# Performance work log

Hardware: AMD Instinct MI355X
Metric: run time of the kernel (lower is better)

Reference implementation:

```python
import jax, jax.numpy as jnp
import numpy as np

NUM_HEADS = 16
HEAD_DIM = 64  # dim // num_heads


def setup_inputs() -> dict:
    key = jax.random.key(0)
    ks = jax.random.split(key, 4)
    B, N, C = 16, 4096, 1024
    s = 0.02
    x = jax.random.normal(ks[0], (B, N, C), dtype=jnp.float32)
    Wq = jax.random.normal(ks[1], (C, NUM_HEADS * HEAD_DIM), dtype=jnp.float32) * s
    Wkv = jax.random.normal(ks[2], (C, NUM_HEADS * HEAD_DIM * 2), dtype=jnp.float32) * s
    Wproj = jax.random.normal(ks[3], (NUM_HEADS * HEAD_DIM, C), dtype=jnp.float32) * s
    bproj = jnp.zeros((C,), dtype=jnp.float32)
    return {"x": x, "Wq": Wq, "Wkv": Wkv, "Wproj": Wproj, "bproj": bproj}


def reference(x, Wq, Wkv, Wproj, bproj):
    B, N, C = x.shape
    H, D = NUM_HEADS, HEAD_DIM
    scale = D ** (-0.5)
    # k, v projections over the full sequence: [B, N, 2, H, D]
    kv = (x @ Wkv).reshape(B, N, 2, H, D)
    k = kv[:, :, 0]  # [B, N, H, D]
    v = kv[:, :, 1]  # [B, N, H, D]
    # query from CLS token only: [B, 1, H, D]
    q = (x[:, :1, :] @ Wq).reshape(B, 1, H, D)
    # decode-style attention: single query attends over N keys
    attn = jnp.einsum("bqhd,bnhd->bhqn", q * scale, k)  # [B, H, 1, N]
    attn = jax.nn.softmax(attn, axis=-1)
    cls_embed = jnp.einsum("bhqn,bnhd->bqhd", attn, v).reshape(B, 1, H * D)
    return cls_embed @ Wproj + bproj  # [B, 1, C]
```

## Files before the change

kernel.cpp:

```cpp
#include <hip/hip_runtime.h>
#include <cstddef>
#include <cstdint>

#define B_ 16
#define N_ 4096
#define C_ 1024
#define H_ 16
#define D_ 64
#define HD_ 1024

__device__ __forceinline__ void stage16(const float* g, float* l, int lane) {
#if __has_builtin(__builtin_amdgcn_global_load_lds)
  __builtin_amdgcn_global_load_lds(
      (const __attribute__((address_space(1))) void*)g,
      (__attribute__((address_space(3))) void*)l, 16, 0, 0);
#else
  *(float4*)(l + lane * 4) = *(const float4*)g;
#endif
}

__global__ __launch_bounds__(256) void kA(const float* __restrict__ x,
                                          const float* __restrict__ Wq,
                                          const float* __restrict__ Wkv,
                                          float* __restrict__ u) {
  const int b = blockIdx.x >> 4;
  const int h = blockIdx.x & 15;
  __shared__ float xr[C_];
  __shared__ float qp[4][D_];
  __shared__ float qs[D_];
  const float* xb = x + (size_t)b * N_ * C_;
  for (int c = threadIdx.x; c < C_; c += 256) xr[c] = xb[c];
  __syncthreads();
  const int d = threadIdx.x & 63;
  const int part = threadIdx.x >> 6;
  float a = 0.f;
  const float* wq = Wq + h * D_ + d;
  #pragma unroll 4
  for (int c = part * 256; c < part * 256 + 256; ++c)
    a += xr[c] * wq[(size_t)c * HD_];
  qp[part][d] = a;
  __syncthreads();
  if (threadIdx.x < 64) {
    qs[threadIdx.x] = (qp[0][threadIdx.x] + qp[1][threadIdx.x] +
                       qp[2][threadIdx.x] + qp[3][threadIdx.x]) * 0.125f;
  }
  __syncthreads();
  for (int c = threadIdx.x; c < C_; c += 256) {
    const float4* wr = (const float4*)(Wkv + (size_t)c * (2 * HD_) + h * D_);
    float s = 0.f;
    #pragma unroll
    for (int d4 = 0; d4 < 16; ++d4) {
      float4 wv = wr[d4];
      s += wv.x * qs[4 * d4] + wv.y * qs[4 * d4 + 1] +
           wv.z * qs[4 * d4 + 2] + wv.w * qs[4 * d4 + 3];
    }
    u[(size_t)blockIdx.x * C_ + c] = s;
  }
}

__global__ __launch_bounds__(256, 2) void kF(const float* __restrict__ x,
                                             const float* __restrict__ u,
                                             float* __restrict__ wpart,
                                             float* __restrict__ mbuf,
                                             float* __restrict__ lbuf,
                                             int G) {
  const int b = blockIdx.y;
  const int chunk = blockIdx.x;
  const int CH = gridDim.x;
  const int tid = threadIdx.x;
  const int w = tid >> 6;
  const int lane = tid & 63;
  __shared__ float xs[2][8][C_];

  float4 uf[4][4];
  const float* ub = u + (size_t)(b * H_ + w * 4) * C_;
  #pragma unroll
  for (int hh = 0; hh < 4; ++hh)
    #pragma unroll
    for (int q = 0; q < 4; ++q)
      uf[hh][q] = *(const float4*)(ub + (size_t)hh * C_ + q * 256 + lane * 4);

  float4 acc[4][4];
  #pragma unroll
  for (int hh = 0; hh < 4; ++hh)
    #pragma unroll
    for (int q = 0; q < 4; ++q) acc[hh][q] = make_float4(0.f, 0.f, 0.f, 0.f);
  float m[4] = {-1e30f, -1e30f, -1e30f, -1e30f};
  float l[4] = {0.f, 0.f, 0.f, 0.f};

  const float* xb = x + ((size_t)b * N_ + (size_t)chunk * G * 8) * C_;

  #pragma unroll
  for (int r = 0; r < 8; ++r)
    stage16(xb + (size_t)r * C_ + w * 256 + lane * 4, &xs[0][r][w * 256], lane);

  for (int g = 0; g < G; ++g) {
    __syncthreads();
    if (g + 1 < G) {
      const float* xg = xb + (size_t)(g + 1) * 8 * C_;
      const int nb = (g + 1) & 1;
      #pragma unroll
      for (int r = 0; r < 8; ++r)
        stage16(xg + (size_t)r * C_ + w * 256 + lane * 4, &xs[nb][r][w * 256],
                lane);
    }
    const int buf = g & 1;
    #pragma unroll
    for (int r = 0; r < 8; ++r) {
      float4 xq[4];
      #pragma unroll
      for (int q = 0; q < 4; ++q)
        xq[q] = *(const float4*)&xs[buf][r][q * 256 + lane * 4];
      float ph[4];
      #pragma unroll
      for (int hh = 0; hh < 4; ++hh) {
        float a = 0.f;
        #pragma unroll
        for (int q = 0; q < 4; ++q)
          a += xq[q].x * uf[hh][q].x + xq[q].y * uf[hh][q].y +
               xq[q].z * uf[hh][q].z + xq[q].w * uf[hh][q].w;
        ph[hh] = a;
      }
      #pragma unroll
      for (int mask = 1; mask < 64; mask <<= 1) {
        #pragma unroll
        for (int hh = 0; hh < 4; ++hh) ph[hh] += __shfl_xor(ph[hh], mask);
      }
      float mn[4];
      #pragma unroll
      for (int hh = 0; hh < 4; ++hh) mn[hh] = fmaxf(m[hh], ph[hh]);
      if (mn[0] > m[0] || mn[1] > m[1] || mn[2] > m[2] || mn[3] > m[3]) {
        #pragma unroll
        for (int hh = 0; hh < 4; ++hh) {
          const float alpha = __expf(m[hh] - mn[hh]);
          l[hh] *= alpha;
          #pragma unroll
          for (int q = 0; q < 4; ++q) {
            acc[hh][q].x *= alpha; acc[hh][q].y *= alpha;
            acc[hh][q].z *= alpha; acc[hh][q].w *= alpha;
          }
          m[hh] = mn[hh];
        }
      }
      #pragma unroll
      for (int hh = 0; hh < 4; ++hh) {
        const float p = __expf(ph[hh] - m[hh]);
        l[hh] += p;
        #pragma unroll
        for (int q = 0; q < 4; ++q) {
          acc[hh][q].x += p * xq[q].x; acc[hh][q].y += p * xq[q].y;
          acc[hh][q].z += p * xq[q].z; acc[hh][q].w += p * xq[q].w;
        }
      }
    }
  }

  float* wp = wpart + ((size_t)(b * CH + chunk) * H_ + w * 4) * C_;
  #pragma unroll
  for (int hh = 0; hh < 4; ++hh)
    #pragma unroll
    for (int q = 0; q < 4; ++q)
      *(float4*)(wp + (size_t)hh * C_ + q * 256 + lane * 4) = acc[hh][q];
  if (lane == 0) {
    #pragma unroll
    for (int hh = 0; hh < 4; ++hh) {
      mbuf[(b * CH + chunk) * H_ + w * 4 + hh] = m[hh];
      lbuf[(b * CH + chunk) * H_ + w * 4 + hh] = l[hh];
    }
  }
}

__global__ __launch_bounds__(256) void kM(const float* __restrict__ wpart,
                                          const float* __restrict__ mbuf,
                                          const float* __restrict__ lbuf,
                                          float* __restrict__ w, int CH) {
  const int b = blockIdx.x >> 4;
  const int h = blockIdx.x & 15;
  const int t = threadIdx.x;
  __shared__ float alph[64];
  __shared__ float Linv;
  if (t < 64) {
    float mv = (t < CH) ? mbuf[(b * CH + t) * H_ + h] : -1e30f;
    float M = mv;
    #pragma unroll
    for (int mask = 1; mask < 64; mask <<= 1)
      M = fmaxf(M, __shfl_xor(M, mask));
    const float lv = (t < CH) ? lbuf[(b * CH + t) * H_ + h] : 0.f;
    const float a = __expf(mv - M);
    alph[t] = a;
    float L = a * lv;
    #pragma unroll
    for (int mask = 1; mask < 64; mask <<= 1) L += __shfl_xor(L, mask);
    if (t == 0) Linv = 1.f / L;
  }
  __syncthreads();
  float4 sum = make_float4(0.f, 0.f, 0.f, 0.f);
  for (int s = 0; s < CH; ++s) {
    const float a = alph[s];
    const float4 v =
        *(const float4*)(wpart + ((size_t)(b * CH + s) * H_ + h) * C_ + t * 4);
    sum.x += a * v.x; sum.y += a * v.y; sum.z += a * v.z; sum.w += a * v.w;
  }
  const float li = Linv;
  float4 o = make_float4(sum.x * li, sum.y * li, sum.z * li, sum.w * li);
  *(float4*)(w + (size_t)(b * H_ + h) * C_ + t * 4) = o;
}

__global__ __launch_bounds__(256) void kE1(const float* __restrict__ w,
                                           const float* __restrict__ Wkv,
                                           float* __restrict__ cls) {
  const int b = blockIdx.x >> 4;
  const int g = blockIdx.x & 15;
  const int t = threadIdx.x;
  const int j = t & 63;
  const int part = t >> 6;
  const float* wr = w + (size_t)(b * H_ + g) * C_ + part * 256;
  const float* wv = Wkv + 1024 + g * 64 + j;
  float acc = 0.f;
  #pragma unroll 8
  for (int c = 0; c < 256; ++c)
    acc += wr[c] * wv[(size_t)(part * 256 + c) * 2048];
  __shared__ float red[256];
  red[t] = acc;
  __syncthreads();
  if (t < 64) {
    const float s = red[t] + red[t + 64] + red[t + 128] + red[t + 192];
    cls[(size_t)b * HD_ + g * 64 + t] = s;
  }
}

__global__ __launch_bounds__(256) void kE2(const float* __restrict__ cls,
                                           const float* __restrict__ Wproj,
                                           const float* __restrict__ bproj,
                                           float* __restrict__ out) {
  const int b = blockIdx.x >> 4;
  const int g = blockIdx.x & 15;
  const int t = threadIdx.x;
  const int j = g * 64 + (t & 63);
  const int part = t >> 6;
  const float* cb = cls + (size_t)b * HD_ + part * 256;
  float acc = 0.f;
  #pragma unroll 8
  for (int i = 0; i < 256; ++i)
    acc += cb[i] * Wproj[(size_t)(part * 256 + i) * C_ + j];
  __shared__ float red[256];
  red[t] = acc;
  __syncthreads();
  if (t < 64) {
    const float s =
        red[t] + red[t + 64] + red[t + 128] + red[t + 192] + bproj[g * 64 + t];
    out[(size_t)b * C_ + g * 64 + t] = s;
  }
}

extern "C" void kernel_launch(void* const* d_in, const int* in_sizes, int n_in,
                              void* d_out, int out_size, void* d_ws,
                              size_t ws_size, hipStream_t stream) {
  const float* x = (const float*)d_in[0];
  const float* Wq = (const float*)d_in[1];
  const float* Wkv = (const float*)d_in[2];
  const float* Wproj = (const float*)d_in[3];
  const float* bproj = (const float*)d_in[4];
  float* ws = (float*)d_ws;

  int CH = 64;
  for (;;) {
    size_t fl = 262144ull + (size_t)CH * 262144ull + 2ull * CH * 256ull +
                262144ull + 16384ull;
    if (fl * 4ull <= ws_size || CH == 8) break;
    CH >>= 1;
  }
  const int G = N_ / (CH * 8);

  float* u = ws;
  float* wpart = u + 262144;
  float* mbuf = wpart + (size_t)CH * 262144ull;
  float* lbuf = mbuf + (size_t)CH * 256ull;
  float* w = lbuf + (size_t)CH * 256ull;
  float* cls = w + 262144;

  kA<<<dim3(B_ * H_), dim3(256), 0, stream>>>(x, Wq, Wkv, u);
  kF<<<dim3(CH, B_), dim3(256), 0, stream>>>(x, u, wpart, mbuf, lbuf, G);
  kM<<<dim3(256), dim3(256), 0, stream>>>(wpart, mbuf, lbuf, w, CH);
  kE1<<<dim3(256), dim3(256), 0, stream>>>(w, Wkv, cls);
  kE2<<<dim3(256), dim3(256), 0, stream>>>(cls, Wproj, bproj, (float*)d_out);
}
```

Baseline: 514.3 us.

## Drop online-softmax max tracking and merge chunk partials with atomics

```diff
diff --git a/kernel.cpp b/kernel.cpp
--- a/kernel.cpp
+++ b/kernel.cpp
@@ -8,6 +8,8 @@
 #define H_ 16
 #define D_ 64
 #define HD_ 1024
+#define CH_ 64
+#define G_ 8
 
 __device__ __forceinline__ void stage16(const float* g, float* l, int lane) {
 #if __has_builtin(__builtin_amdgcn_global_load_lds)
@@ -19,33 +21,52 @@
 #endif
 }
 
-__global__ __launch_bounds__(256) void kA(const float* __restrict__ x,
+__device__ __forceinline__ void atomAddF(float* p, float v) {
+  __hip_atomic_fetch_add(p, v, __ATOMIC_RELAXED, __HIP_MEMORY_SCOPE_AGENT);
+}
+
+__global__ __launch_bounds__(512) void kA(const float* __restrict__ x,
                                           const float* __restrict__ Wq,
                                           const float* __restrict__ Wkv,
-                                          float* __restrict__ u) {
+                                          float* __restrict__ u,
+                                          float* __restrict__ wun,
+                                          float* __restrict__ L,
+                                          float* __restrict__ cls) {
   const int b = blockIdx.x >> 4;
   const int h = blockIdx.x & 15;
+  const int t = threadIdx.x;
   __shared__ float xr[C_];
-  __shared__ float qp[4][D_];
+  __shared__ float qp[8][D_];
   __shared__ float qs[D_];
+
+  {
+    float* wz = wun + (size_t)blockIdx.x * C_;
+    for (int c = t; c < C_; c += 512) wz[c] = 0.f;
+    if (t < 64) cls[(size_t)b * HD_ + h * 64 + t] = 0.f;
+    if (t == 0) L[blockIdx.x] = 0.f;
+  }
+
   const float* xb = x + (size_t)b * N_ * C_;
-  for (int c = threadIdx.x; c < C_; c += 256) xr[c] = xb[c];
-  __syncthreads();
-  const int d = threadIdx.x & 63;
-  const int part = threadIdx.x >> 6;
+  for (int c = t; c < C_; c += 512) xr[c] = xb[c];
+  __syncthreads();
+
+  const int d = t & 63;
+  const int part = t >> 6;
   float a = 0.f;
   const float* wq = Wq + h * D_ + d;
-  #pragma unroll 4
-  for (int c = part * 256; c < part * 256 + 256; ++c)
+  #pragma unroll 8
+  for (int c = part * 128; c < part * 128 + 128; ++c)
     a += xr[c] * wq[(size_t)c * HD_];
   qp[part][d] = a;
   __syncthreads();
-  if (threadIdx.x < 64) {
-    qs[threadIdx.x] = (qp[0][threadIdx.x] + qp[1][threadIdx.x] +
-                       qp[2][threadIdx.x] + qp[3][threadIdx.x]) * 0.125f;
-  }
-  __syncthreads();
-  for (int c = threadIdx.x; c < C_; c += 256) {
+  if (t < 64) {
+    float s = 0.f;
+    #pragma unroll
+    for (int p = 0; p < 8; ++p) s += qp[p][t];
+    qs[t] = s * 0.125f;
+  }
+  __syncthreads();
+  for (int c = t; c < C_; c += 512) {
     const float4* wr = (const float4*)(Wkv + (size_t)c * (2 * HD_) + h * D_);
     float s = 0.f;
     #pragma unroll
@@ -58,50 +79,46 @@
   }
 }
 
-__global__ __launch_bounds__(256, 2) void kF(const float* __restrict__ x,
+__global__ __launch_bounds__(512, 4) void kF(const float* __restrict__ x,
                                              const float* __restrict__ u,
-                                             float* __restrict__ wpart,
-                                             float* __restrict__ mbuf,
-                                             float* __restrict__ lbuf,
-                                             int G) {
+                                             float* __restrict__ wun,
+                                             float* __restrict__ L) {
   const int b = blockIdx.y;
   const int chunk = blockIdx.x;
-  const int CH = gridDim.x;
   const int tid = threadIdx.x;
   const int w = tid >> 6;
   const int lane = tid & 63;
   __shared__ float xs[2][8][C_];
 
-  float4 uf[4][4];
-  const float* ub = u + (size_t)(b * H_ + w * 4) * C_;
-  #pragma unroll
-  for (int hh = 0; hh < 4; ++hh)
+  float4 uf[2][4];
+  const float* ub = u + (size_t)(b * H_ + w * 2) * C_;
+  #pragma unroll
+  for (int hh = 0; hh < 2; ++hh)
     #pragma unroll
     for (int q = 0; q < 4; ++q)
       uf[hh][q] = *(const float4*)(ub + (size_t)hh * C_ + q * 256 + lane * 4);
 
-  float4 acc[4][4];
-  #pragma unroll
-  for (int hh = 0; hh < 4; ++hh)
+  float4 acc[2][4];
+  #pragma unroll
+  for (int hh = 0; hh < 2; ++hh)
     #pragma unroll
     for (int q = 0; q < 4; ++q) acc[hh][q] = make_float4(0.f, 0.f, 0.f, 0.f);
-  float m[4] = {-1e30f, -1e30f, -1e30f, -1e30f};
-  float l[4] = {0.f, 0.f, 0.f, 0.f};
-
-  const float* xb = x + ((size_t)b * N_ + (size_t)chunk * G * 8) * C_;
-
-  #pragma unroll
-  for (int r = 0; r < 8; ++r)
-    stage16(xb + (size_t)r * C_ + w * 256 + lane * 4, &xs[0][r][w * 256], lane);
-
-  for (int g = 0; g < G; ++g) {
+  float lsum = 0.f;
+
+  const float* xb = x + ((size_t)b * N_ + (size_t)chunk * 64) * C_;
+
+  #pragma unroll
+  for (int q = 0; q < 4; ++q)
+    stage16(xb + (size_t)w * C_ + q * 256 + lane * 4, &xs[0][w][q * 256], lane);
+
+  for (int g = 0; g < G_; ++g) {
     __syncthreads();
-    if (g + 1 < G) {
+    if (g + 1 < G_) {
       const float* xg = xb + (size_t)(g + 1) * 8 * C_;
       const int nb = (g + 1) & 1;
       #pragma unroll
-      for (int r = 0; r < 8; ++r)
-        stage16(xg + (size_t)r * C_ + w * 256 + lane * 4, &xs[nb][r][w * 256],
+      for (int q = 0; q < 4; ++q)
+        stage16(xg + (size_t)w * C_ + q * 256 + lane * 4, &xs[nb][w][q * 256],
                 lane);
     }
     const int buf = g & 1;
@@ -111,125 +128,81 @@
       #pragma unroll
       for (int q = 0; q < 4; ++q)
         xq[q] = *(const float4*)&xs[buf][r][q * 256 + lane * 4];
-      float ph[4];
-      #pragma unroll
-      for (int hh = 0; hh < 4; ++hh) {
-        float a = 0.f;
-        #pragma unroll
-        for (int q = 0; q < 4; ++q)
-          a += xq[q].x * uf[hh][q].x + xq[q].y * uf[hh][q].y +
-               xq[q].z * uf[hh][q].z + xq[q].w * uf[hh][q].w;
-        ph[hh] = a;
+      float p0 = 0.f, p1 = 0.f;
+      #pragma unroll
+      for (int q = 0; q < 4; ++q) {
+        p0 += xq[q].x * uf[0][q].x + xq[q].y * uf[0][q].y +
+              xq[q].z * uf[0][q].z + xq[q].w * uf[0][q].w;
+        p1 += xq[q].x * uf[1][q].x + xq[q].y * uf[1][q].y +
+              xq[q].z * uf[1][q].z + xq[q].w * uf[1][q].w;
       }
-      #pragma unroll
-      for (int mask = 1; mask < 64; mask <<= 1) {
-        #pragma unroll
-        for (int hh = 0; hh < 4; ++hh) ph[hh] += __shfl_xor(ph[hh], mask);
+      const bool odd = lane & 1;
+      float keep = odd ? p1 : p0;
+      float send = odd ? p0 : p1;
+      float y = keep + __shfl_xor(send, 1);
+      y += __shfl_xor(y, 2);
+      y += __shfl_xor(y, 4);
+      y += __shfl_xor(y, 8);
+      y += __shfl_xor(y, 16);
+      y += __shfl_xor(y, 32);
+      const float e = __expf(y);
+      lsum += e;
+      const float eo = __shfl_xor(e, 1);
+      const float pe0 = odd ? eo : e;
+      const float pe1 = odd ? e : eo;
+      #pragma unroll
+      for (int q = 0; q < 4; ++q) {
+        acc[0][q].x += pe0 * xq[q].x; acc[0][q].y += pe0 * xq[q].y;
+        acc[0][q].z += pe0 * xq[q].z; acc[0][q].w += pe0 * xq[q].w;
+        acc[1][q].x += pe1 * xq[q].x; acc[1][q].y += pe1 * xq[q].y;
+        acc[1][q].z += pe1 * xq[q].z; acc[1][q].w += pe1 * xq[q].w;
       }
-      float mn[4];
-      #pragma unroll
-      for (int hh = 0; hh < 4; ++hh) mn[hh] = fmaxf(m[hh], ph[hh]);
-      if (mn[0] > m[0] || mn[1] > m[1] || mn[2] > m[2] || mn[3] > m[3]) {
-        #pragma unroll
-        for (int hh = 0; hh < 4; ++hh) {
-          const float alpha = __expf(m[hh] - mn[hh]);
-          l[hh] *= alpha;
-          #pragma unroll
-          for (int q = 0; q < 4; ++q) {
-            acc[hh][q].x *= alpha; acc[hh][q].y *= alpha;
-            acc[hh][q].z *= alpha; acc[hh][q].w *= alpha;
-          }
-          m[hh] = mn[hh];
-        }
-      }
-      #pragma unroll
-      for (int hh = 0; hh < 4; ++hh) {
-        const float p = __expf(ph[hh] - m[hh]);
-        l[hh] += p;
-        #pragma unroll
-        for (int q = 0; q < 4; ++q) {
-          acc[hh][q].x += p * xq[q].x; acc[hh][q].y += p * xq[q].y;
-          acc[hh][q].z += p * xq[q].z; acc[hh][q].w += p * xq[q].w;
-        }
-      }
-    }
-  }
-
-  float* wp = wpart + ((size_t)(b * CH + chunk) * H_ + w * 4) * C_;
-  #pragma unroll
-  for (int hh = 0; hh < 4; ++hh)
-    #pragma unroll
-    for (int q = 0; q < 4; ++q)
-      *(float4*)(wp + (size_t)hh * C_ + q * 256 + lane * 4) = acc[hh][q];
-  if (lane == 0) {
-    #pragma unroll
-    for (int hh = 0; hh < 4; ++hh) {
-      mbuf[(b * CH + chunk) * H_ + w * 4 + hh] = m[hh];
-      lbuf[(b * CH + chunk) * H_ + w * 4 + hh] = l[hh];
-    }
-  }
-}
-
-__global__ __launch_bounds__(256) void kM(const float* __restrict__ wpart,
-                                          const float* __restrict__ mbuf,
-                                          const float* __restrict__ lbuf,
-                                          float* __restrict__ w, int CH) {
-  const int b = blockIdx.x >> 4;
-  const int h = blockIdx.x & 15;
-  const int t = threadIdx.x;
-  __shared__ float alph[64];
-  __shared__ float Linv;
-  if (t < 64) {
-    float mv = (t < CH) ? mbuf[(b * CH + t) * H_ + h] : -1e30f;
-    float M = mv;
-    #pragma unroll
-    for (int mask = 1; mask < 64; mask <<= 1)
-      M = fmaxf(M, __shfl_xor(M, mask));
-    const float lv = (t < CH) ? lbuf[(b * CH + t) * H_ + h] : 0.f;
-    const float a = __expf(mv - M);
-    alph[t] = a;
-    float L = a * lv;
-    #pragma unroll
-    for (int mask = 1; mask < 64; mask <<= 1) L += __shfl_xor(L, mask);
-    if (t == 0) Linv = 1.f / L;
-  }
-  __syncthreads();
-  float4 sum = make_float4(0.f, 0.f, 0.f, 0.f);
-  for (int s = 0; s < CH; ++s) {
-    const float a = alph[s];
-    const float4 v =
-        *(const float4*)(wpart + ((size_t)(b * CH + s) * H_ + h) * C_ + t * 4);
-    sum.x += a * v.x; sum.y += a * v.y; sum.z += a * v.z; sum.w += a * v.w;
-  }
-  const float li = Linv;
-  float4 o = make_float4(sum.x * li, sum.y * li, sum.z * li, sum.w * li);
-  *(float4*)(w + (size_t)(b * H_ + h) * C_ + t * 4) = o;
-}
-
-__global__ __launch_bounds__(256) void kE1(const float* __restrict__ w,
+    }
+  }
+
+  float* wp = wun + (size_t)(b * H_ + w * 2) * C_;
+  #pragma unroll
+  for (int hh = 0; hh < 2; ++hh)
+    #pragma unroll
+    for (int q = 0; q < 4; ++q) {
+      float* dst = wp + (size_t)hh * C_ + q * 256 + lane * 4;
+      atomAddF(dst + 0, acc[hh][q].x);
+      atomAddF(dst + 1, acc[hh][q].y);
+      atomAddF(dst + 2, acc[hh][q].z);
+      atomAddF(dst + 3, acc[hh][q].w);
+    }
+  if (lane < 2) atomAddF(&L[b * H_ + w * 2 + lane], lsum);
+}
+
+__global__ __launch_bounds__(256) void kE1(const float* __restrict__ wun,
                                            const float* __restrict__ Wkv,
                                            float* __restrict__ cls) {
-  const int b = blockIdx.x >> 4;
-  const int g = blockIdx.x & 15;
+  const int bh = blockIdx.x >> 2;
+  const int b = bh >> 4;
+  const int h = bh & 15;
+  const int qr = blockIdx.x & 3;
   const int t = threadIdx.x;
   const int j = t & 63;
-  const int part = t >> 6;
-  const float* wr = w + (size_t)(b * H_ + g) * C_ + part * 256;
-  const float* wv = Wkv + 1024 + g * 64 + j;
+  const int sub = t >> 6;
+  __shared__ float wsh[256];
+  __shared__ float red[256];
+  wsh[t] = wun[(size_t)bh * C_ + qr * 256 + t];
+  __syncthreads();
+  const float* wv = Wkv + HD_ + h * D_ + j;
+  const int cbase = qr * 256 + sub * 64;
   float acc = 0.f;
-  #pragma unroll 8
-  for (int c = 0; c < 256; ++c)
-    acc += wr[c] * wv[(size_t)(part * 256 + c) * 2048];
-  __shared__ float red[256];
+  #pragma unroll 16
+  for (int i = 0; i < 64; ++i)
+    acc += wsh[sub * 64 + i] * wv[(size_t)(cbase + i) * (2 * HD_)];
   red[t] = acc;
   __syncthreads();
-  if (t < 64) {
-    const float s = red[t] + red[t + 64] + red[t + 128] + red[t + 192];
-    cls[(size_t)b * HD_ + g * 64 + t] = s;
-  }
-}
-
-__global__ __launch_bounds__(256) void kE2(const float* __restrict__ cls,
+  if (t < 64)
+    atomAddF(&cls[(size_t)b * HD_ + h * 64 + t],
+             red[t] + red[t + 64] + red[t + 128] + red[t + 192]);
+}
+
+__global__ __launch_bounds__(512) void kE2(const float* __restrict__ cls,
+                                           const float* __restrict__ L,
                                            const float* __restrict__ Wproj,
                                            const float* __restrict__ bproj,
                                            float* __restrict__ out) {
@@ -238,17 +211,25 @@
   const int t = threadIdx.x;
   const int j = g * 64 + (t & 63);
   const int part = t >> 6;
-  const float* cb = cls + (size_t)b * HD_ + part * 256;
+  __shared__ float Li[H_];
+  __shared__ float csc[HD_];
+  __shared__ float red[512];
+  if (t < H_) Li[t] = 1.f / L[b * H_ + t];
+  __syncthreads();
+  csc[t] = cls[(size_t)b * HD_ + t] * Li[t >> 6];
+  csc[t + 512] = cls[(size_t)b * HD_ + t + 512] * Li[(t + 512) >> 6];
+  __syncthreads();
+  const int i0 = part * 128;
   float acc = 0.f;
-  #pragma unroll 8
-  for (int i = 0; i < 256; ++i)
-    acc += cb[i] * Wproj[(size_t)(part * 256 + i) * C_ + j];
-  __shared__ float red[256];
+  #pragma unroll 16
+  for (int i = 0; i < 128; ++i)
+    acc += csc[i0 + i] * Wproj[(size_t)(i0 + i) * C_ + j];
   red[t] = acc;
   __syncthreads();
   if (t < 64) {
-    const float s =
-        red[t] + red[t + 64] + red[t + 128] + red[t + 192] + bproj[g * 64 + t];
+    float s = bproj[g * 64 + t];
+    #pragma unroll
+    for (int p = 0; p < 8; ++p) s += red[p * 64 + t];
     out[(size_t)b * C_ + g * 64 + t] = s;
   }
 }
@@ -263,25 +244,14 @@
   const float* bproj = (const float*)d_in[4];
   float* ws = (float*)d_ws;
 
-  int CH = 64;
-  for (;;) {
-    size_t fl = 262144ull + (size_t)CH * 262144ull + 2ull * CH * 256ull +
-                262144ull + 16384ull;
-    if (fl * 4ull <= ws_size || CH == 8) break;
-    CH >>= 1;
-  }
-  const int G = N_ / (CH * 8);
-
   float* u = ws;
-  float* wpart = u + 262144;
-  float* mbuf = wpart + (size_t)CH * 262144ull;
-  float* lbuf = mbuf + (size_t)CH * 256ull;
-  float* w = lbuf + (size_t)CH * 256ull;
-  float* cls = w + 262144;
-
-  kA<<<dim3(B_ * H_), dim3(256), 0, stream>>>(x, Wq, Wkv, u);
-  kF<<<dim3(CH, B_), dim3(256), 0, stream>>>(x, u, wpart, mbuf, lbuf, G);
-  kM<<<dim3(256), dim3(256), 0, stream>>>(wpart, mbuf, lbuf, w, CH);
-  kE1<<<dim3(256), dim3(256), 0, stream>>>(w, Wkv, cls);
-  kE2<<<dim3(256), dim3(256), 0, stream>>>(cls, Wproj, bproj, (float*)d_out);
-}
+  float* wun = u + 262144;
+  float* L = wun + 262144;
+  float* cls = L + 256;
+
+  kA<<<dim3(B_ * H_), dim3(512), 0, stream>>>(x, Wq, Wkv, u, wun, L, cls);
+  kF<<<dim3(CH_, B_), dim3(512), 0, stream>>>(x, u, wun, L);
+  kE1<<<dim3(B_ * H_ * 4), dim3(256), 0, stream>>>(wun, Wkv, cls);
+  kE2<<<dim3(B_ * H_), dim3(512), 0, stream>>>(cls, L, Wproj, bproj,
+                                               (float*)d_out);
+}
```

After: 787.4 us. 53.1% more time.
